# Optimization experiments

Hardware: AMD Instinct MI355X
Metric: run time of the kernel (lower is better)

## Reference

```python
import jax, jax.numpy as jnp
import numpy as np
import math

FACTOR = 5  # args.factor


def setup_inputs() -> dict:
    key = jax.random.key(0)
    kq, kk, kv, ki = jax.random.split(key, 4)
    B, L, H, D = 8, 2048, 8, 64
    sample_k = min(FACTOR * int(np.ceil(np.log(L))), L)  # 40
    return {
        "queries": jax.random.normal(kq, (B, L, H, D), dtype=jnp.float32),
        "keys": jax.random.normal(kk, (B, L, H, D), dtype=jnp.float32),
        "values": jax.random.normal(kv, (B, L, H, D), dtype=jnp.float32),
        "index_sample": jax.random.randint(ki, (L, sample_k), 0, L),
    }


def reference(queries, keys, values, index_sample):
    B, L_Q, H, D = queries.shape
    L_K = keys.shape[1]
    # [B, L, H, D] -> [B, H, L, D]
    Q = queries.transpose(0, 2, 1, 3)
    K = keys.transpose(0, 2, 1, 3)
    V = values.transpose(0, 2, 1, 3)

    u = min(FACTOR * int(np.ceil(np.log(L_Q))), L_Q)  # n_top

    # ---- _prob_QK: sampled scores + sparsity measure + top-u queries ----
    # gather sampled keys per query position: [B, H, L_Q, sample_k, D]
    K_sample = K[:, :, index_sample, :]
    Q_K_sample = jnp.einsum('bhqd,bhqsd->bhqs', Q, K_sample)  # [B,H,L_Q,S]
    M = Q_K_sample.max(-1) - Q_K_sample.mean(-1)              # [B,H,L_Q]
    _, M_top = jax.lax.top_k(M, u)                            # [B,H,u]

    Q_reduce = jnp.take_along_axis(Q, M_top[..., None], axis=2)  # [B,H,u,D]
    scores = jnp.einsum('bhud,bhkd->bhuk', Q_reduce, K) * (1.0 / math.sqrt(D))

    # ---- initial context: mean of V broadcast over queries ----
    context = jnp.broadcast_to(V.mean(axis=2, keepdims=True), (B, H, L_Q, D))

    # ---- update context at selected query positions ----
    attn = jax.nn.softmax(scores, axis=-1)                  # [B,H,u,L_K]
    ctx_upd = jnp.einsum('bhuk,bhkd->bhud', attn, V)        # [B,H,u,D]
    bi = jnp.arange(B)[:, None, None]
    hi = jnp.arange(H)[None, :, None]
    context = context.at[bi, hi, M_top].set(ctx_upd)

    # [B,H,L_Q,D] -> [B,L_Q,H*D]
    return context.transpose(0, 2, 1, 3).reshape(B, L_Q, H * D)
```

## Files before the change

kernel.cpp:

```cpp
#include <hip/hip_runtime.h>
#include <hip/hip_bf16.h>

#define BB 8
#define LL 2048
#define HH 8
#define DD 64
#define HD 512
#define SK 40
#define UU 40
#define NCHUNK 16
#define CHUNK 128

typedef float v4f __attribute__((ext_vector_type(4)));

static const size_t OFF_M     = 0;
static const size_t OFF_TOP   = 512ull * 1024;
static const size_t OFF_VPART = 592ull * 1024;
static const size_t OFF_MPART = 768ull * 1024;
static const size_t OFF_SPART = 960ull * 1024;
static const size_t OFF_OPART = 1152ull * 1024;

template <int CTRL>
__device__ __forceinline__ float dpp_add(float x) {
    int yi = __builtin_amdgcn_mov_dpp(__float_as_int(x), CTRL, 0xF, 0xF, true);
    return x + __int_as_float(yi);
}

__global__ __launch_bounds__(128) void kA_sample_scores(
    const float* __restrict__ Q, const float* __restrict__ K,
    const int* __restrict__ IS, float* __restrict__ M)
{
    int blk = blockIdx.x;
    int b = blk & 7;
    int q = blk >> 3;
    int tid = threadIdx.x;
    int h = tid >> 4;
    int lane = tid & 15;

    const int* __restrict__ isq = IS + q * SK;
    size_t base = (size_t)b * LL * HD;
    int off = h * DD + lane * 4;
    v4f qv = __builtin_nontemporal_load(
        (const v4f*)(Q + base + (size_t)q * HD + off));
    const float* __restrict__ Kb = K + base;

    float mx = -1e30f, sm = 0.f;
#pragma unroll 16
    for (int s = 0; s < SK; ++s) {
        int idx = __builtin_amdgcn_readfirstlane(isq[s]);
        const float* __restrict__ Krow = Kb + (size_t)idx * HD;
        const float4 kv = *(const float4*)(Krow + off);
        float p = qv.x * kv.x + qv.y * kv.y + qv.z * kv.z + qv.w * kv.w;
        p = dpp_add<0xB1>(p);
        p = dpp_add<0x4E>(p);
        p = dpp_add<0x141>(p);
        p = dpp_add<0x140>(p);
        mx = fmaxf(mx, p);
        sm += p;
    }
    if (lane == 0)
        M[((size_t)(b * HH + h)) * LL + q] = mx - sm * (1.0f / SK);
}

__global__ __launch_bounds__(256) void kB_topk(
    const float* __restrict__ M, int* __restrict__ TopIdx)
{
    int bh = blockIdx.x;
    int tid = threadIdx.x;
    __shared__ unsigned keys[LL];
    __shared__ int      hist[4096];
    __shared__ int      sscan[256];
    __shared__ unsigned ckeyA[2048];
    __shared__ int      cidxA[2048];
    __shared__ unsigned ckeyB[2048];
    __shared__ int      cidxB[2048];
    __shared__ int ctr[8];

    const float* __restrict__ m = M + (size_t)bh * LL;
    for (int i = tid; i < 4096; i += 256) hist[i] = 0;
    if (tid < 8) ctr[tid] = 0;
    __syncthreads();

    for (int i = tid; i < LL; i += 256) {
        unsigned u = __float_as_uint(m[i]);
        u = (u & 0x80000000u) ? ~u : (u | 0x80000000u);
        keys[i] = u;
        atomicAdd(&hist[u >> 20], 1);
    }
    __syncthreads();
    {
        int p = 0;
#pragma unroll
        for (int j = 0; j < 16; ++j) p += hist[tid * 16 + j];
        sscan[tid] = p;
        __syncthreads();
        for (int o = 1; o < 256; o <<= 1) {
            int v = (tid + o < 256) ? sscan[tid + o] : 0;
            __syncthreads();
            sscan[tid] += v;
            __syncthreads();
        }
        int snext = (tid < 255) ? sscan[tid + 1] : 0;
        if (sscan[tid] >= UU && snext < UU) {
            int cum = snext;
            for (int bkt = tid * 16 + 15; bkt >= tid * 16; --bkt) {
                int c = hist[bkt];
                if (cum + c >= UU) { ctr[3] = bkt; ctr[4] = UU - cum; break; }
                cum += c;
            }
        }
    }
    __syncthreads();
    unsigned T1 = (unsigned)ctr[3];
    int k1 = ctr[4];
    for (int i = tid; i < LL; i += 256) {
        unsigned u = keys[i];
        unsigned bkt = u >> 20;
        if (bkt > T1) {
            int p = atomicAdd(&ctr[0], 1);
            TopIdx[bh * UU + p] = i;
        } else if (bkt == T1) {
            int p = atomicAdd(&ctr[1], 1);
            ckeyA[p] = u; cidxA[p] = i;
        }
    }
    __syncthreads();
    int nA = ctr[1];

    for (int i = tid; i < 4096; i += 256) hist[i] = 0;
    __syncthreads();
    for (int i = tid; i < nA; i += 256)
        atomicAdd(&hist[(ckeyA[i] >> 8) & 0xFFF], 1);
    __syncthreads();
    {
        int p = 0;
#pragma unroll
        for (int j = 0; j < 16; ++j) p += hist[tid * 16 + j];
        sscan[tid] = p;
        __syncthreads();
        for (int o = 1; o < 256; o <<= 1) {
            int v = (tid + o < 256) ? sscan[tid + o] : 0;
            __syncthreads();
            sscan[tid] += v;
            __syncthreads();
        }
        int snext = (tid < 255) ? sscan[tid + 1] : 0;
        if (sscan[tid] >= k1 && snext < k1) {
            int cum = snext;
            for (int bkt = tid * 16 + 15; bkt >= tid * 16; --bkt) {
                int c = hist[bkt];
                if (cum + c >= k1) { ctr[3] = bkt; ctr[4] = k1 - cum; break; }
                cum += c;
            }
        }
    }
    __syncthreads();
    unsigned T2 = (unsigned)ctr[3];
    int k2 = ctr[4];
    for (int i = tid; i < nA; i += 256) {
        unsigned u = ckeyA[i];
        unsigned bkt = (u >> 8) & 0xFFF;
        if (bkt > T2) {
            int p = atomicAdd(&ctr[0], 1);
            TopIdx[bh * UU + p] = cidxA[i];
        } else if (bkt == T2) {
            int p = atomicAdd(&ctr[2], 1);
            ckeyB[p] = u; cidxB[p] = cidxA[i];
        }
    }
    __syncthreads();
    int nB = ctr[2];

    for (int i = tid; i < 256; i += 256) hist[i] = 0;
    __syncthreads();
    for (int i = tid; i < nB; i += 256)
        atomicAdd(&hist[ckeyB[i] & 0xFF], 1);
    __syncthreads();
    {
        sscan[tid] = hist[tid];
        __syncthreads();
        for (int o = 1; o < 256; o <<= 1) {
            int v = (tid + o < 256) ? sscan[tid + o] : 0;
            __syncthreads();
            sscan[tid] += v;
            __syncthreads();
        }
        int snext = (tid < 255) ? sscan[tid + 1] : 0;
        if (sscan[tid] >= k2 && snext < k2) { ctr[3] = tid; ctr[4] = k2 - snext; }
    }
    __syncthreads();
    unsigned T3 = (unsigned)ctr[3];
    int k3 = ctr[4];
    for (int i = tid; i < nB; i += 256) {
        unsigned u = ckeyB[i];
        unsigned bkt = u & 0xFF;
        if (bkt > T3) {
            int p = atomicAdd(&ctr[0], 1);
            TopIdx[bh * UU + p] = cidxB[i];
        } else if (bkt == T3) {
            int p = atomicAdd(&ctr[5], 1);
            cidxA[p] = cidxB[i];
        }
    }
    __syncthreads();
    if (tid == 0) {
        int n = ctr[5];
        int basep = ctr[0];
        for (int r = 0; r < k3; ++r) {
            int bi = 1 << 30, bp = -1;
            for (int j = 0; j < n; ++j) {
                int id = cidxA[j];
                if (id >= 0 && id < bi) { bi = id; bp = j; }
            }
            TopIdx[bh * UU + basep + r] = bi;
            cidxA[bp] = -1;
        }
    }
}

__global__ __launch_bounds__(256) void kC_vmean(
    const float* __restrict__ V, float* __restrict__ Vpart)
{
    int bh = blockIdx.x >> 3;
    int ch = blockIdx.x & 7;
    int b = bh >> 3, h = bh & 7;
    int tid = threadIdx.x;
    int dq = tid & 15;
    int lg = tid >> 4;

    float4 acc = make_float4(0.f, 0.f, 0.f, 0.f);
    size_t base = ((size_t)b * LL + ch * 256) * HD + h * DD + dq * 4;
    for (int l = lg; l < 256; l += 16) {
        float4 v = *(const float4*)(V + base + (size_t)l * HD);
        acc.x += v.x; acc.y += v.y; acc.z += v.z; acc.w += v.w;
    }
    __shared__ float4 red[256];
    red[tid] = acc;
    __syncthreads();
    if (tid < 16) {
        float4 s = make_float4(0.f, 0.f, 0.f, 0.f);
#pragma unroll
        for (int g = 0; g < 16; ++g) {
            float4 v = red[g * 16 + tid];
            s.x += v.x; s.y += v.y; s.z += v.z; s.w += v.w;
        }
        *(float4*)(Vpart + ch * 4096 + bh * 64 + tid * 4) = s;
    }
}

__global__ __launch_bounds__(256) void kD_fill(
    const float* __restrict__ Vpart, float* __restrict__ out)
{
    size_t i4 = (size_t)blockIdx.x * 256 + threadIdx.x;
    size_t o = i4 * 4;
    int hd = (int)(o & (HD - 1));
    int b  = (int)(o >> 20);
    int h  = hd >> 6;
    int idx = (b * HH + h) * DD + (hd & 63);
    float4 acc = make_float4(0.f, 0.f, 0.f, 0.f);
#pragma unroll
    for (int c = 0; c < 8; ++c) {
        float4 v = *(const float4*)(Vpart + c * 4096 + idx);
        acc.x += v.x; acc.y += v.y; acc.z += v.z; acc.w += v.w;
    }
    const float sc = 1.0f / LL;
    float4 r; r.x = acc.x * sc; r.y = acc.y * sc; r.z = acc.z * sc; r.w = acc.w * sc;
    *(float4*)(out + o) = r;
}

__global__ __launch_bounds__(256) void kE_attn_partial(
    const float* __restrict__ Q, const float* __restrict__ K, const float* __restrict__ V,
    const int* __restrict__ TopIdx,
    float* __restrict__ Opart, float* __restrict__ mpart, float* __restrict__ spart)
{
    int c  = blockIdx.x;
    int bh = blockIdx.y;
    int b = bh >> 3, h = bh & 7;
    int tid = threadIdx.x;

    __shared__ float Qs[UU * DD];
    __shared__ float P[CHUNK * 41];
    __shared__ int   qidx[UU];
    __shared__ float wmax[2][UU];
    __shared__ float wsum[2][UU];
    __shared__ float mred[UU], sred[UU];

    if (tid < UU) qidx[tid] = TopIdx[bh * UU + tid];
    __syncthreads();

    size_t hbase  = (size_t)b * LL * HD + h * DD;
    size_t kcbase = hbase + (size_t)c * CHUNK * HD;

    for (int r = tid; r < UU * 16; r += 256) {
        int u = r >> 4, j = r & 15;
        *(float4*)(Qs + u * DD + j * 4) =
            *(const float4*)(Q + hbase + (size_t)qidx[u] * HD + j * 4);
    }
    __syncthreads();

    {
        int l = tid & (CHUNK - 1), ug = tid >> 7;
        int pair = (tid >> 6) & 1;
        const float* __restrict__ Krow = K + kcbase + (size_t)l * HD;
        float dot[20];
#pragma unroll
        for (int i = 0; i < 20; ++i) dot[i] = 0.f;

#pragma unroll
        for (int half = 0; half < 2; ++half) {
            float4 kr[8];
#pragma unroll
            for (int j = 0; j < 8; ++j)
                kr[j] = *(const float4*)(Krow + half * 32 + j * 4);
#pragma unroll
            for (int j = 0; j < 8; ++j) {
                float4 kv = kr[j];
#pragma unroll
                for (int uu = 0; uu < 20; ++uu) {
                    float4 qv = *(const float4*)(Qs + (ug * 20 + uu) * DD + half * 32 + j * 4);
                    dot[uu] += kv.x * qv.x + kv.y * qv.y + kv.z * qv.z + kv.w * qv.w;
                }
            }
        }

        float wm[20];
#pragma unroll
        for (int uu = 0; uu < 20; ++uu) {
            float d = dot[uu] * 0.125f;
            dot[uu] = d;
            float v = d;
            v = fmaxf(v, __shfl_xor(v, 1));
            v = fmaxf(v, __shfl_xor(v, 2));
            v = fmaxf(v, __shfl_xor(v, 4));
            v = fmaxf(v, __shfl_xor(v, 8));
            v = fmaxf(v, __shfl_xor(v, 16));
            v = fmaxf(v, __shfl_xor(v, 32));
            wm[uu] = v;
        }
        if ((tid & 63) == 0) {
#pragma unroll
            for (int uu = 0; uu < 20; ++uu) wmax[pair][ug * 20 + uu] = wm[uu];
        }
        __syncthreads();

        float ws[20];
#pragma unroll
        for (int uu = 0; uu < 20; ++uu) {
            int u = ug * 20 + uu;
            float m = fmaxf(wmax[0][u], wmax[1][u]);
            float p = __expf(dot[uu] - m);
            dot[uu] = m;
            P[l * 41 + u] = p;
            float v = p;
            v += __shfl_xor(v, 1);
            v += __shfl_xor(v, 2);
            v += __shfl_xor(v, 4);
            v += __shfl_xor(v, 8);
            v += __shfl_xor(v, 16);
            v += __shfl_xor(v, 32);
            ws[uu] = v;
        }
        if ((tid & 63) == 0) {
#pragma unroll
            for (int uu = 0; uu < 20; ++uu) wsum[pair][ug * 20 + uu] = ws[uu];
        }
        __syncthreads();

        if (tid == 0 || tid == 128) {
#pragma unroll
            for (int uu = 0; uu < 20; ++uu) {
                int u = ug * 20 + uu;
                mred[u] = dot[uu];
                sred[u] = wsum[0][u] + wsum[1][u];
            }
        }
    }

    {
        int dq = tid & 15, ug4 = tid >> 4;
        float4 acc[3];
#pragma unroll
        for (int i = 0; i < 3; ++i) acc[i] = make_float4(0.f, 0.f, 0.f, 0.f);
        const float* __restrict__ Vb = V + kcbase + dq * 4;
        for (int l0 = 0; l0 < CHUNK; l0 += 8) {
            float4 v[8];
#pragma unroll
            for (int j = 0; j < 8; ++j)
                v[j] = *(const float4*)(Vb + (size_t)(l0 + j) * HD);
#pragma unroll
            for (int j = 0; j < 8; ++j) {
#pragma unroll
                for (int i = 0; i < 3; ++i) {
                    int u = ug4 + 16 * i;
                    if (u < UU) {
                        float p = P[(l0 + j) * 41 + u];
                        acc[i].x += p * v[j].x; acc[i].y += p * v[j].y;
                        acc[i].z += p * v[j].z; acc[i].w += p * v[j].w;
                    }
                }
            }
        }
#pragma unroll
        for (int i = 0; i < 3; ++i) {
            int u = ug4 + 16 * i;
            if (u < UU) {
                size_t ob = (((size_t)(bh * UU + u)) * NCHUNK + c) * DD + dq * 4;
                *(float4*)(Opart + ob) = acc[i];
            }
        }
    }
    __syncthreads();
    if (tid < UU) {
        mpart[(bh * UU + tid) * NCHUNK + c] = mred[tid];
        spart[(bh * UU + tid) * NCHUNK + c] = sred[tid];
    }
}

__global__ __launch_bounds__(64) void kF_combine(
    const float* __restrict__ Opart, const float* __restrict__ mpart,
    const float* __restrict__ spart, const int* __restrict__ TopIdx,
    float* __restrict__ out)
{
    int g = blockIdx.x;
    int bh = g / UU;
    int b = bh >> 3, h = bh & 7;
    int d = threadIdx.x;

    float m_i[NCHUNK];
    float Mx = -1e30f;
#pragma unroll
    for (int i = 0; i < NCHUNK; ++i) { m_i[i] = mpart[g * NCHUNK + i]; Mx = fmaxf(Mx, m_i[i]); }
    float S = 0.f, O = 0.f;
#pragma unroll
    for (int i = 0; i < NCHUNK; ++i) {
        float w = __expf(m_i[i] - Mx);
        S += w * spart[g * NCHUNK + i];
        O += w * Opart[((size_t)g * NCHUNK + i) * DD + d];
    }
    int qi = TopIdx[g];
    out[((size_t)b * LL + qi) * HD + h * DD + d] = O / S;
}

extern "C" void kernel_launch(void* const* d_in, const int* in_sizes, int n_in,
                              void* d_out, int out_size, void* d_ws, size_t ws_size,
                              hipStream_t stream) {
    const float* Q  = (const float*)d_in[0];
    const float* K  = (const float*)d_in[1];
    const float* V  = (const float*)d_in[2];
    const int*   IS = (const int*)d_in[3];
    float* out = (float*)d_out;
    char* ws = (char*)d_ws;

    float* M      = (float*)(ws + OFF_M);
    int*   TopIdx = (int*)(ws + OFF_TOP);
    float* Vpart  = (float*)(ws + OFF_VPART);
    float* mpart  = (float*)(ws + OFF_MPART);
    float* spart  = (float*)(ws + OFF_SPART);
    float* Opart  = (float*)(ws + OFF_OPART);

    kA_sample_scores<<<BB * LL, 128, 0, stream>>>(Q, K, IS, M);
    kC_vmean<<<BB * HH * 8, 256, 0, stream>>>(V, Vpart);
    kB_topk<<<BB * HH, 256, 0, stream>>>(M, TopIdx);
    kD_fill<<<(BB * LL * HD) / (256 * 4), 256, 0, stream>>>(Vpart, out);
    kE_attn_partial<<<dim3(NCHUNK, BB * HH), 256, 0, stream>>>(Q, K, V, TopIdx,
                                                               Opart, mpart, spart);
    kF_combine<<<BB * HH * UU, 64, 0, stream>>>(Opart, mpart, spart, TopIdx, out);
}
```

Baseline: 251.7 us.

## Restructure attention partial QK/softmax mapping and prefetch sampled K rows

The sampled-score kernel now resolves all sample indices up front and keeps a rolling register prefetch of K rows, so gather latency overlaps with the dot products. The attention-partial kernel now gives each wavefront 10 queries over two 64-key halves, which lets the softmax max and sum be reduced within one wavefront and removes two block-wide barriers and the cross-wave shared buffers. Probabilities are stored transposed (query-major, padded), so the PV loop reads them as float4 vectors instead of scalar loads. The costs are more register pressure and different LDS bank access patterns.

```diff
diff --git a/kernel.cpp b/kernel.cpp
--- a/kernel.cpp
+++ b/kernel.cpp
@@ -26,7 +26,8 @@
     return x + __int_as_float(yi);
 }
 
-__global__ __launch_bounds__(128) void kA_sample_scores(
+#define KA_PF 10
+__global__ __launch_bounds__(128, 4) void kA_sample_scores(
     const float* __restrict__ Q, const float* __restrict__ K,
     const int* __restrict__ IS, float* __restrict__ M)
 {
@@ -44,13 +45,23 @@
         (const v4f*)(Q + base + (size_t)q * HD + off));
     const float* __restrict__ Kb = K + base;
 
+    int sidx[SK];
+#pragma unroll
+    for (int s = 0; s < SK; ++s)
+        sidx[s] = __builtin_amdgcn_readfirstlane(isq[s]);
+
+    float4 kv[KA_PF];
+#pragma unroll
+    for (int i = 0; i < KA_PF; ++i)
+        kv[i] = *(const float4*)(Kb + (size_t)sidx[i] * HD + off);
+
     float mx = -1e30f, sm = 0.f;
-#pragma unroll 16
+#pragma unroll
     for (int s = 0; s < SK; ++s) {
-        int idx = __builtin_amdgcn_readfirstlane(isq[s]);
-        const float* __restrict__ Krow = Kb + (size_t)idx * HD;
-        const float4 kv = *(const float4*)(Krow + off);
-        float p = qv.x * kv.x + qv.y * kv.y + qv.z * kv.z + qv.w * kv.w;
+        float4 k = kv[s % KA_PF];
+        if (s + KA_PF < SK)
+            kv[s % KA_PF] = *(const float4*)(Kb + (size_t)sidx[s + KA_PF] * HD + off);
+        float p = qv.x * k.x + qv.y * k.y + qv.z * k.z + qv.w * k.w;
         p = dpp_add<0xB1>(p);
         p = dpp_add<0x4E>(p);
         p = dpp_add<0x141>(p);
@@ -279,10 +290,8 @@
     int tid = threadIdx.x;
 
     __shared__ float Qs[UU * DD];
-    __shared__ float P[CHUNK * 41];
+    __shared__ float PT[UU][CHUNK + 4];
     __shared__ int   qidx[UU];
-    __shared__ float wmax[2][UU];
-    __shared__ float wsum[2][UU];
     __shared__ float mred[UU], sred[UU];
 
     if (tid < UU) qidx[tid] = TopIdx[bh * UU + tid];
@@ -299,82 +308,61 @@
     __syncthreads();
 
     {
-        int l = tid & (CHUNK - 1), ug = tid >> 7;
-        int pair = (tid >> 6) & 1;
-        const float* __restrict__ Krow = K + kcbase + (size_t)l * HD;
-        float dot[20];
-#pragma unroll
-        for (int i = 0; i < 20; ++i) dot[i] = 0.f;
-
-#pragma unroll
-        for (int half = 0; half < 2; ++half) {
-            float4 kr[8];
-#pragma unroll
-            for (int j = 0; j < 8; ++j)
-                kr[j] = *(const float4*)(Krow + half * 32 + j * 4);
-#pragma unroll
-            for (int j = 0; j < 8; ++j) {
-                float4 kv = kr[j];
-#pragma unroll
-                for (int uu = 0; uu < 20; ++uu) {
-                    float4 qv = *(const float4*)(Qs + (ug * 20 + uu) * DD + half * 32 + j * 4);
-                    dot[uu] += kv.x * qv.x + kv.y * qv.y + kv.z * qv.z + kv.w * qv.w;
+        int w = tid >> 6;
+        int lane = tid & 63;
+        const float* __restrict__ K0 = K + kcbase + (size_t)lane * HD;
+        const float* __restrict__ K1 = K0 + (size_t)64 * HD;
+
+        float d0[10], d1[10];
+#pragma unroll
+        for (int i = 0; i < 10; ++i) { d0[i] = 0.f; d1[i] = 0.f; }
+
+#pragma unroll
+        for (int qt = 0; qt < 4; ++qt) {
+            float4 ka[4], kb[4];
+#pragma unroll
+            for (int j = 0; j < 4; ++j) {
+                ka[j] = *(const float4*)(K0 + qt * 16 + j * 4);
+                kb[j] = *(const float4*)(K1 + qt * 16 + j * 4);
+            }
+#pragma unroll
+            for (int j = 0; j < 4; ++j) {
+#pragma unroll
+                for (int uu = 0; uu < 10; ++uu) {
+                    float4 qv = *(const float4*)(Qs + (w * 10 + uu) * DD + qt * 16 + j * 4);
+                    d0[uu] += qv.x * ka[j].x + qv.y * ka[j].y + qv.z * ka[j].z + qv.w * ka[j].w;
+                    d1[uu] += qv.x * kb[j].x + qv.y * kb[j].y + qv.z * kb[j].z + qv.w * kb[j].w;
                 }
             }
         }
 
-        float wm[20];
-#pragma unroll
-        for (int uu = 0; uu < 20; ++uu) {
-            float d = dot[uu] * 0.125f;
-            dot[uu] = d;
-            float v = d;
-            v = fmaxf(v, __shfl_xor(v, 1));
-            v = fmaxf(v, __shfl_xor(v, 2));
-            v = fmaxf(v, __shfl_xor(v, 4));
-            v = fmaxf(v, __shfl_xor(v, 8));
-            v = fmaxf(v, __shfl_xor(v, 16));
-            v = fmaxf(v, __shfl_xor(v, 32));
-            wm[uu] = v;
-        }
-        if ((tid & 63) == 0) {
-#pragma unroll
-            for (int uu = 0; uu < 20; ++uu) wmax[pair][ug * 20 + uu] = wm[uu];
-        }
-        __syncthreads();
-
-        float ws[20];
-#pragma unroll
-        for (int uu = 0; uu < 20; ++uu) {
-            int u = ug * 20 + uu;
-            float m = fmaxf(wmax[0][u], wmax[1][u]);
-            float p = __expf(dot[uu] - m);
-            dot[uu] = m;
-            P[l * 41 + u] = p;
-            float v = p;
-            v += __shfl_xor(v, 1);
-            v += __shfl_xor(v, 2);
-            v += __shfl_xor(v, 4);
-            v += __shfl_xor(v, 8);
-            v += __shfl_xor(v, 16);
-            v += __shfl_xor(v, 32);
-            ws[uu] = v;
-        }
-        if ((tid & 63) == 0) {
-#pragma unroll
-            for (int uu = 0; uu < 20; ++uu) wsum[pair][ug * 20 + uu] = ws[uu];
-        }
-        __syncthreads();
-
-        if (tid == 0 || tid == 128) {
-#pragma unroll
-            for (int uu = 0; uu < 20; ++uu) {
-                int u = ug * 20 + uu;
-                mred[u] = dot[uu];
-                sred[u] = wsum[0][u] + wsum[1][u];
-            }
-        }
-    }
+#pragma unroll
+        for (int uu = 0; uu < 10; ++uu) {
+            int u = w * 10 + uu;
+            float x0 = d0[uu] * 0.125f;
+            float x1 = d1[uu] * 0.125f;
+            float m = fmaxf(x0, x1);
+            m = fmaxf(m, __shfl_xor(m, 1));
+            m = fmaxf(m, __shfl_xor(m, 2));
+            m = fmaxf(m, __shfl_xor(m, 4));
+            m = fmaxf(m, __shfl_xor(m, 8));
+            m = fmaxf(m, __shfl_xor(m, 16));
+            m = fmaxf(m, __shfl_xor(m, 32));
+            float p0 = __expf(x0 - m);
+            float p1 = __expf(x1 - m);
+            PT[u][lane]      = p0;
+            PT[u][lane + 64] = p1;
+            float s = p0 + p1;
+            s += __shfl_xor(s, 1);
+            s += __shfl_xor(s, 2);
+            s += __shfl_xor(s, 4);
+            s += __shfl_xor(s, 8);
+            s += __shfl_xor(s, 16);
+            s += __shfl_xor(s, 32);
+            if (lane == 0) { mred[u] = m; sred[u] = s; }
+        }
+    }
+    __syncthreads();
 
     {
         int dq = tid & 15, ug4 = tid >> 4;
@@ -388,15 +376,19 @@
             for (int j = 0; j < 8; ++j)
                 v[j] = *(const float4*)(Vb + (size_t)(l0 + j) * HD);
 #pragma unroll
-            for (int j = 0; j < 8; ++j) {
-#pragma unroll
-                for (int i = 0; i < 3; ++i) {
-                    int u = ug4 + 16 * i;
-                    if (u < UU) {
-                        float p = P[(l0 + j) * 41 + u];
-                        acc[i].x += p * v[j].x; acc[i].y += p * v[j].y;
-                        acc[i].z += p * v[j].z; acc[i].w += p * v[j].w;
-                    }
+            for (int i = 0; i < 3; ++i) {
+                int u = ug4 + 16 * i;
+                if (u < UU) {
+                    float4 pa = *(const float4*)(&PT[u][l0]);
+                    float4 pb = *(const float4*)(&PT[u][l0 + 4]);
+                    acc[i].x += pa.x * v[0].x + pa.y * v[1].x + pa.z * v[2].x + pa.w * v[3].x
+                              + pb.x * v[4].x + pb.y * v[5].x + pb.z * v[6].x + pb.w * v[7].x;
+                    acc[i].y += pa.x * v[0].y + pa.y * v[1].y + pa.z * v[2].y + pa.w * v[3].y
+                              + pb.x * v[4].y + pb.y * v[5].y + pb.z * v[6].y + pb.w * v[7].y;
+                    acc[i].z += pa.x * v[0].z + pa.y * v[1].z + pa.z * v[2].z + pa.w * v[3].z
+                              + pb.x * v[4].z + pb.y * v[5].z + pb.z * v[6].z + pb.w * v[7].z;
+                    acc[i].w += pa.x * v[0].w + pa.y * v[1].w + pa.z * v[2].w + pa.w * v[3].w
+                              + pb.x * v[4].w + pb.y * v[5].w + pb.z * v[6].w + pb.w * v[7].w;
                 }
             }
         }
@@ -409,7 +401,6 @@
             }
         }
     }
-    __syncthreads();
     if (tid < UU) {
         mpart[(bh * UU + tid) * NCHUNK + c] = mred[tid];
         spart[(bh * UU + tid) * NCHUNK + c] = sred[tid];
```

Result: slower. 372.2 us (+47.9%).
